# Optimization experiments

Hardware: AMD Instinct MI355X
Metric: run time of the kernel (lower is better)

The kernel has to match this reference:

```python
import jax, jax.numpy as jnp
import numpy as np

N = 50000   # nodes
E = 800000  # edges
D = 64      # num_filters == hidden_channels
NG = 5      # num_gaussians (edge_attr width, unused by forward math)
NEG_SLOPE = 0.2


def setup_inputs() -> dict:
    key = jax.random.key(0)
    ks = jax.random.split(key, 16)
    s = 1.0 / np.sqrt(D)
    return {
        "x": jax.random.normal(ks[0], (N, D), dtype=jnp.float32),
        "edge_index": jax.random.randint(ks[1], (2, E), 0, N, dtype=jnp.int64),
        "edge_weight": jax.random.uniform(ks[2], (E,), dtype=jnp.float32),
        "edge_attr": jax.random.normal(ks[3], (E, NG), dtype=jnp.float32),
        "W0": jax.random.normal(ks[4], (D, D), dtype=jnp.float32) * s,
        "b0": jnp.zeros((D,), dtype=jnp.float32),
        "W1": jax.random.normal(ks[5], (D, D), dtype=jnp.float32) * s,
        "as1": jax.random.normal(ks[6], (D,), dtype=jnp.float32) * s,
        "ad1": jax.random.normal(ks[7], (D,), dtype=jnp.float32) * s,
        "b1": jnp.zeros((D,), dtype=jnp.float32),
        "W2": jax.random.normal(ks[8], (D, D), dtype=jnp.float32) * s,
        "as2": jax.random.normal(ks[9], (D,), dtype=jnp.float32) * s,
        "ad2": jax.random.normal(ks[10], (D,), dtype=jnp.float32) * s,
        "b2": jnp.zeros((D,), dtype=jnp.float32),
    }


def gat_layer(h, src, dst, W, a_src, a_dst, b):
    # PyG GATConv, heads=1, add_self_loops=False
    hx = h @ W  # [N, D]
    # per-node attention logits, gathered per edge (edge j->i: src=j, dst=i)
    alpha = (hx * a_src).sum(-1)[src] + (hx * a_dst).sum(-1)[dst]  # [E]
    alpha = jax.nn.leaky_relu(alpha, NEG_SLOPE)
    # segment softmax grouped by destination node
    m = jax.ops.segment_max(alpha, dst, num_segments=N)
    e = jnp.exp(alpha - m[dst])
    s = jax.ops.segment_sum(e, dst, num_segments=N)
    p = e / s[dst]  # [E]
    # scatter-add weighted source features
    out = jax.ops.segment_sum(hx[src] * p[:, None], dst, num_segments=N)
    return out + b


def reference(x, edge_index, edge_weight, edge_attr,
              W0, b0, W1, as1, ad1, b1, W2, as2, ad2, b2):
    # edge_weight / edge_attr are accepted but unused, as in the torch module
    src, dst = edge_index[0], edge_index[1]
    out = jax.nn.relu(x @ W0 + b0)
    out = out + jax.nn.relu(gat_layer(out, src, dst, W1, as1, ad1, b1))
    out = out + jax.nn.relu(gat_layer(out, src, dst, W2, as2, ad2, b2))
    return out
```

## Files before the change

### kernel.cpp

```cpp
#include <hip/hip_runtime.h>

#define DD 64
#define NEG_SLOPE 0.2f
#define HS 68
#define CAP 64
#define BSH 8
#define BN  256
#define NBMAX 256
#define NBLK 256
#define CAPB 6144
#define STAGE_CAP 6144
#define AMM_NODES 32
#define CWS 65

__device__ __forceinline__ unsigned short f2bf(float f)
{
    unsigned u = __float_as_uint(f);
    u += 0x7FFFu + ((u >> 16) & 1u);
    return (unsigned short)(u >> 16);
}
__device__ __forceinline__ float bf2f(unsigned short b)
{
    return __uint_as_float(((unsigned)b) << 16);
}

__device__ __forceinline__ int wave_incl_scan(int v, int lane)
{
#pragma unroll
    for (int off = 1; off < 64; off <<= 1) {
        int t = __shfl_up(v, off);
        if (lane >= off) v += t;
    }
    return v;
}

__device__ __forceinline__ void group_aggregate(
    const ushort4* __restrict__ hx, const int* __restrict__ col,
    const float* __restrict__ sarr, float adi, int beg, int deg, int fl,
    uint2* __restrict__ cw, float4& acc, float& s)
{
    s = 0.f;
    acc = float4{0.f, 0.f, 0.f, 0.f};

#define GATH(P) { float wv = __uint_as_float((P).y);                          \
                  ushort4 uu = hx[(P).x * 16 + fl];                           \
                  acc.x += wv * bf2f(uu.x); acc.y += wv * bf2f(uu.y);         \
                  acc.z += wv * bf2f(uu.z); acc.w += wv * bf2f(uu.w); }

    if (deg <= CAP) {
        int c0 = 0, c1 = 0, c2 = 0, c3 = 0;
        float w0 = 0.f, w1 = 0.f, w2 = 0.f, w3 = 0.f;
        if (fl < deg)      { c0 = col[beg + fl];      float a = sarr[c0] + adi; a = a > 0.f ? a : NEG_SLOPE * a; w0 = __expf(a); }
        if (fl + 16 < deg) { c1 = col[beg + fl + 16]; float a = sarr[c1] + adi; a = a > 0.f ? a : NEG_SLOPE * a; w1 = __expf(a); }
        if (fl + 32 < deg) { c2 = col[beg + fl + 32]; float a = sarr[c2] + adi; a = a > 0.f ? a : NEG_SLOPE * a; w2 = __expf(a); }
        if (fl + 48 < deg) { c3 = col[beg + fl + 48]; float a = sarr[c3] + adi; a = a > 0.f ? a : NEG_SLOPE * a; w3 = __expf(a); }
        s = (w0 + w1) + (w2 + w3);

        int degR = (deg + 7) & ~7;
        if (fl < degR)      { uint2 e; e.x = (unsigned)c0; e.y = __float_as_uint(w0); cw[fl] = e; }
        if (fl + 16 < degR) { uint2 e; e.x = (unsigned)c1; e.y = __float_as_uint(w1); cw[fl + 16] = e; }
        if (fl + 32 < degR) { uint2 e; e.x = (unsigned)c2; e.y = __float_as_uint(w2); cw[fl + 32] = e; }
        if (fl + 48 < degR) { uint2 e; e.x = (unsigned)c3; e.y = __float_as_uint(w3); cw[fl + 48] = e; }

        for (int i = 0; i < degR; i += 8) {
            uint2 p0 = cw[i],     p1 = cw[i + 1], p2 = cw[i + 2], p3 = cw[i + 3];
            uint2 p4 = cw[i + 4], p5 = cw[i + 5], p6 = cw[i + 6], p7 = cw[i + 7];
            GATH(p0); GATH(p1); GATH(p2); GATH(p3);
            GATH(p4); GATH(p5); GATH(p6); GATH(p7);
        }
    } else {
        for (int base = 0; base < deg; base += 16) {
            int i = base + fl;
            uint2 e; e.x = 0u; e.y = 0u;
            if (i < deg) {
                int c = col[beg + i];
                float a = sarr[c] + adi;
                a = a > 0.f ? a : NEG_SLOPE * a;
                float wv = __expf(a);
                e.x = (unsigned)c; e.y = __float_as_uint(wv);
                s += wv;
            }
            cw[fl] = e;
#pragma unroll
            for (int j = 0; j < 16; j += 8) {
                uint2 p0 = cw[j],     p1 = cw[j + 1], p2 = cw[j + 2], p3 = cw[j + 3];
                uint2 p4 = cw[j + 4], p5 = cw[j + 5], p6 = cw[j + 6], p7 = cw[j + 7];
                GATH(p0); GATH(p1); GATH(p2); GATH(p3);
                GATH(p4); GATH(p5); GATH(p6); GATH(p7);
            }
        }
    }
#pragma unroll
    for (int off = 8; off; off >>= 1) s += __shfl_xor(s, off);
#undef GATH
}

__global__ __launch_bounds__(512) void scatter_mm(
    const int4* __restrict__ dst4, const int4* __restrict__ src4,
    const int* __restrict__ dst, const int* __restrict__ src,
    int* __restrict__ gcur, int* __restrict__ ebuf,
    int NB, int E4, int E, int C4,
    const float* __restrict__ x, const float* __restrict__ W0,
    const float* __restrict__ b0, const float* __restrict__ W1,
    const float* __restrict__ a_src, const float* __restrict__ a_dst,
    float* __restrict__ h, ushort4* __restrict__ hxb4,
    float* __restrict__ sarr, float* __restrict__ darr, int n)
{
    __shared__ float smem[DD * DD + DD * HS];
    int tid = threadIdx.x;

    if (blockIdx.x < NBLK) {
        int* lh   = (int*)smem;
        int* lcur = lh + NBMAX;
        int k = blockIdx.x;
        for (int i = tid; i < NB; i += 512) lh[i] = 0;
        __syncthreads();
        int i0 = k * C4, i1 = min(i0 + C4, E4);
        for (int i = i0 + tid; i < i1; i += 512) {
            int4 d = dst4[i];
            atomicAdd(&lh[d.x >> BSH], 1);
            atomicAdd(&lh[d.y >> BSH], 1);
            atomicAdd(&lh[d.z >> BSH], 1);
            atomicAdd(&lh[d.w >> BSH], 1);
        }
        if (k == NBLK - 1) {
            for (int e = E4 * 4 + tid; e < E; e += 512)
                atomicAdd(&lh[dst[e] >> BSH], 1);
        }
        __syncthreads();
        for (int b = tid; b < NB; b += 512) {
            int c = lh[b];
            lcur[b] = b * CAPB + (c ? atomicAdd(&gcur[b], c) : 0);
        }
        __syncthreads();
        for (int i = i0 + tid; i < i1; i += 512) {
            int4 d = dst4[i];
            int4 s = src4[i];
            int b, p;
            b = d.x >> BSH; p = atomicAdd(&lcur[b], 1);
            if (p < b * CAPB + CAPB) ebuf[p] = ((d.x & (BN - 1)) << 24) | s.x;
            b = d.y >> BSH; p = atomicAdd(&lcur[b], 1);
            if (p < b * CAPB + CAPB) ebuf[p] = ((d.y & (BN - 1)) << 24) | s.y;
            b = d.z >> BSH; p = atomicAdd(&lcur[b], 1);
            if (p < b * CAPB + CAPB) ebuf[p] = ((d.z & (BN - 1)) << 24) | s.z;
            b = d.w >> BSH; p = atomicAdd(&lcur[b], 1);
            if (p < b * CAPB + CAPB) ebuf[p] = ((d.w & (BN - 1)) << 24) | s.w;
        }
        if (k == NBLK - 1) {
            for (int e = E4 * 4 + tid; e < E; e += 512) {
                int d = dst[e];
                int b = d >> BSH;
                int p = atomicAdd(&lcur[b], 1);
                if (p < b * CAPB + CAPB)
                    ebuf[p] = ((d & (BN - 1)) << 24) | src[e];
            }
        }
        return;
    }

    float* Wsh = smem;
    float* Hsh = smem + DD * DD;
    int fg = tid & 15, ng = tid >> 4;
    int tile0 = (blockIdx.x - NBLK) * 64;

    for (int i = tid * 4; i < DD * DD; i += 2048)
        *(float4*)&Wsh[i] = *(const float4*)&W0[i];
    for (int p = 0; p < 2; ++p) {
        int nl = p * 32 + ng, gn = tile0 + nl;
        if (gn < n)
            *(float4*)&Hsh[nl * HS + 4 * fg] = *(const float4*)&x[gn * DD + 4 * fg];
    }
    __syncthreads();

    float4 acc[2];
#pragma unroll
    for (int j = 0; j < 2; ++j) acc[j] = float4{0.f, 0.f, 0.f, 0.f};
#pragma unroll 8
    for (int k = 0; k < DD; ++k) {
        float4 w4 = *(float4*)&Wsh[k * DD + 4 * fg];
#pragma unroll
        for (int j = 0; j < 2; ++j) {
            float hv = Hsh[(2 * ng + j) * HS + k];
            acc[j].x += hv * w4.x; acc[j].y += hv * w4.y;
            acc[j].z += hv * w4.z; acc[j].w += hv * w4.w;
        }
    }

    float4 b4 = *(const float4*)&b0[4 * fg];
    float4 o[2];
#pragma unroll
    for (int j = 0; j < 2; ++j) {
        o[j].x = fmaxf(acc[j].x + b4.x, 0.f);
        o[j].y = fmaxf(acc[j].y + b4.y, 0.f);
        o[j].z = fmaxf(acc[j].z + b4.z, 0.f);
        o[j].w = fmaxf(acc[j].w + b4.w, 0.f);
        int gn = tile0 + 2 * ng + j;
        if (gn < n) *(float4*)&h[gn * DD + 4 * fg] = o[j];
    }
    __syncthreads();

#pragma unroll
    for (int j = 0; j < 2; ++j)
        *(float4*)&Hsh[(2 * ng + j) * HS + 4 * fg] = o[j];
    for (int i = tid * 4; i < DD * DD; i += 2048)
        *(float4*)&Wsh[i] = *(const float4*)&W1[i];
    __syncthreads();

#pragma unroll
    for (int j = 0; j < 2; ++j) acc[j] = float4{0.f, 0.f, 0.f, 0.f};
#pragma unroll 8
    for (int k = 0; k < DD; ++k) {
        float4 w4 = *(float4*)&Wsh[k * DD + 4 * fg];
#pragma unroll
        for (int j = 0; j < 2; ++j) {
            float hv = Hsh[(2 * ng + j) * HS + k];
            acc[j].x += hv * w4.x; acc[j].y += hv * w4.y;
            acc[j].z += hv * w4.z; acc[j].w += hv * w4.w;
        }
    }

    float4 as4 = *(const float4*)&a_src[4 * fg];
    float4 ad4 = *(const float4*)&a_dst[4 * fg];
#pragma unroll
    for (int j = 0; j < 2; ++j) {
        int gn = tile0 + 2 * ng + j;
        if (gn < n) {
            ushort4 hb;
            hb.x = f2bf(acc[j].x); hb.y = f2bf(acc[j].y);
            hb.z = f2bf(acc[j].z); hb.w = f2bf(acc[j].w);
            hxb4[gn * 16 + fg] = hb;
        }
        float ps = acc[j].x * as4.x + acc[j].y * as4.y + acc[j].z * as4.z + acc[j].w * as4.w;
        float pd = acc[j].x * ad4.x + acc[j].y * ad4.y + acc[j].z * ad4.z + acc[j].w * ad4.w;
#pragma unroll
        for (int off = 8; off; off >>= 1) {
            ps += __shfl_xor(ps, off);
            pd += __shfl_xor(pd, off);
        }
        if (fg == 0 && gn < n) { sarr[gn] = ps; darr[gn] = pd; }
    }
}

__global__ __launch_bounds__(512) void group_build(
    const int* __restrict__ ebuf, const int* __restrict__ gcur,
    int* __restrict__ row_beg, int* __restrict__ degarr,
    int* __restrict__ col, int N)
{
    __shared__ int lcnt[BN];
    __shared__ int loff[BN];
    __shared__ int lcur[BN];
    __shared__ int wsum[4];
    __shared__ int stage[STAGE_CAP];
    int b = blockIdx.x, tid = threadIdx.x;
    int e0 = b * CAPB;
    int total = min(gcur[b], CAPB);
    int e1 = e0 + total;
    if (tid < BN) { lcnt[tid] = 0; lcur[tid] = 0; }
    __syncthreads();
    for (int e = e0 + tid; e < e1; e += 512)
        atomicAdd(&lcnt[((unsigned)ebuf[e]) >> 24], 1);
    __syncthreads();
    int lane = tid & 63, w = tid >> 6;
    int v = (tid < BN) ? lcnt[tid] : 0;
    int incl = wave_incl_scan(v, lane);
    if (tid < BN && lane == 63) wsum[w] = incl;
    __syncthreads();
    if (tid < BN) {
        int wo = 0;
        for (int i = 0; i < w; ++i) wo += wsum[i];
        int excl = wo + incl - v;
        loff[tid] = excl;
        int node = b * BN + tid;
        if (node < N) { row_beg[node] = e0 + excl; degarr[node] = v; }
    }
    __syncthreads();
    for (int e = e0 + tid; e < e1; e += 512) {
        int p = ebuf[e];
        int dl = ((unsigned)p) >> 24;
        int r = atomicAdd(&lcur[dl], 1);
        stage[loff[dl] + r] = p & 0xFFFFFF;
    }
    __syncthreads();
    for (int i = tid; i < total; i += 512)
        col[e0 + i] = stage[i];
}

__global__ __launch_bounds__(512) void agg_mm(
    const ushort4* __restrict__ hxA, const int* __restrict__ row_beg,
    const int* __restrict__ degarr, const int* __restrict__ col,
    const float* __restrict__ sA, const float* __restrict__ dA,
    const float* __restrict__ bias,
    float* __restrict__ h, const float* __restrict__ W,
    const float* __restrict__ a_src, const float* __restrict__ a_dst,
    ushort4* __restrict__ hxB, float* __restrict__ sB, float* __restrict__ dB,
    int n)
{
    __shared__ float Wsh[DD * DD];
    __shared__ uint2 cwbuf[AMM_NODES][CWS];
    float* Hsh = (float*)&cwbuf[0][0];

    int tid = threadIdx.x;
    int w = tid >> 6, lane = tid & 63, grp = lane >> 4, fl = lane & 15;
    int nl = 4 * w + grp;
    int tile0 = blockIdx.x * AMM_NODES;
    int v = tile0 + nl;
    bool alive = v < n;

    for (int i = tid * 4; i < DD * DD; i += 2048)
        *(float4*)&Wsh[i] = *(const float4*)&W[i];

    int beg = 0, deg = 0;
    float adi = 0.f;
    if (alive) {
        beg = row_beg[v];
        deg = degarr[v];
        adi = dA[v];
    }

    float4 acc; float s;
    group_aggregate(hxA, col, sA, adi, beg, deg, fl, &cwbuf[nl][0], acc, s);

    float4 resid = float4{0.f, 0.f, 0.f, 0.f};
    {
        float inv = (s > 0.f) ? 1.f / s : 0.f;
        float4 b4 = ((const float4*)bias)[fl];
        float4 o;
        o.x = fmaxf(acc.x * inv + b4.x, 0.f);
        o.y = fmaxf(acc.y * inv + b4.y, 0.f);
        o.z = fmaxf(acc.z * inv + b4.z, 0.f);
        o.w = fmaxf(acc.w * inv + b4.w, 0.f);
        if (alive) {
            float4* hp = (float4*)&h[v * DD + 4 * fl];
            float4 cur = *hp;
            cur.x += o.x; cur.y += o.y; cur.z += o.z; cur.w += o.w;
            *hp = cur;
            resid = cur;
        }
    }
    __syncthreads();
    *(float4*)&Hsh[nl * HS + 4 * fl] = resid;
    __syncthreads();

    int nl2 = tid >> 4;
    int fg = tid & 15;
    float4 acc2 = float4{0.f, 0.f, 0.f, 0.f};
#pragma unroll 8
    for (int k = 0; k < DD; ++k) {
        float4 w4 = *(float4*)&Wsh[k * DD + 4 * fg];
        float hv = Hsh[nl2 * HS + k];
        acc2.x += hv * w4.x; acc2.y += hv * w4.y;
        acc2.z += hv * w4.z; acc2.w += hv * w4.w;
    }
    int gn = tile0 + nl2;
    float4 as4 = *(const float4*)&a_src[4 * fg];
    float4 ad4 = *(const float4*)&a_dst[4 * fg];
    if (gn < n) {
        ushort4 hb;
        hb.x = f2bf(acc2.x); hb.y = f2bf(acc2.y);
        hb.z = f2bf(acc2.z); hb.w = f2bf(acc2.w);
        hxB[gn * 16 + fg] = hb;
    }
    float ps = acc2.x * as4.x + acc2.y * as4.y + acc2.z * as4.z + acc2.w * as4.w;
    float pd = acc2.x * ad4.x + acc2.y * ad4.y + acc2.z * ad4.z + acc2.w * ad4.w;
#pragma unroll
    for (int off = 8; off; off >>= 1) {
        ps += __shfl_xor(ps, off);
        pd += __shfl_xor(pd, off);
    }
    if (fg == 0 && gn < n) { sB[gn] = ps; dB[gn] = pd; }
}

__global__ __launch_bounds__(512) void aggregate(
    const ushort4* __restrict__ hxb4, const int* __restrict__ row_beg,
    const int* __restrict__ degarr, const int* __restrict__ col,
    const float* __restrict__ sarr, const float* __restrict__ darr,
    const float* __restrict__ bias, float* __restrict__ h, int n)
{
    __shared__ uint2 cwbuf[AMM_NODES][CWS];
    int tid = threadIdx.x;
    int w = tid >> 6, lane = tid & 63, grp = lane >> 4, fl = lane & 15;
    int nl = 4 * w + grp;
    int v = blockIdx.x * AMM_NODES + nl;
    bool alive = v < n;

    int beg = 0, deg = 0;
    float adi = 0.f;
    if (alive) {
        beg = row_beg[v];
        deg = degarr[v];
        adi = darr[v];
    }

    float4 acc; float s;
    group_aggregate(hxb4, col, sarr, adi, beg, deg, fl, &cwbuf[nl][0], acc, s);

    if (alive) {
        float inv = (s > 0.f) ? 1.f / s : 0.f;
        float4 b4 = ((const float4*)bias)[fl];
        float4 o;
        o.x = fmaxf(acc.x * inv + b4.x, 0.f);
        o.y = fmaxf(acc.y * inv + b4.y, 0.f);
        o.z = fmaxf(acc.z * inv + b4.z, 0.f);
        o.w = fmaxf(acc.w * inv + b4.w, 0.f);
        float4* hp = (float4*)&h[v * DD + 4 * fl];
        float4 cur = *hp;
        cur.x += o.x; cur.y += o.y; cur.z += o.z; cur.w += o.w;
        *hp = cur;
    }
}

extern "C" void kernel_launch(void* const* d_in, const int* in_sizes, int n_in,
                              void* d_out, int out_size, void* d_ws, size_t ws_size,
                              hipStream_t stream)
{
    const float* x  = (const float*)d_in[0];
    const int*   ei = (const int*)d_in[1];
    const float* W0 = (const float*)d_in[4];
    const float* b0 = (const float*)d_in[5];
    const float* W1 = (const float*)d_in[6];
    const float* as1= (const float*)d_in[7];
    const float* ad1= (const float*)d_in[8];
    const float* b1 = (const float*)d_in[9];
    const float* W2 = (const float*)d_in[10];
    const float* as2= (const float*)d_in[11];
    const float* ad2= (const float*)d_in[12];
    const float* b2 = (const float*)d_in[13];

    int N = in_sizes[0] / DD;
    int E = in_sizes[1] / 2;
    int E4 = E >> 2;
    int C4 = (E4 + NBLK - 1) / NBLK;
    int NB = (N + BN - 1) >> BSH;
    float* h = (float*)d_out;

    ushort4* hxA  = (ushort4*)d_ws;
    ushort4* hxB  = hxA + (size_t)N * 16;
    float* sA     = (float*)(hxB + (size_t)N * 16);
    float* dA     = sA + N;
    float* sB     = dA + N;
    float* dB     = sB + N;
    int*   row_beg= (int*)(dB + N);
    int*   degarr = row_beg + N;
    int*   gcur   = degarr + N;
    int*   ebuf   = gcur + NB;
    int*   colb   = ebuf + (size_t)NB * CAPB;

    const int* src = ei;
    const int* dst = ei + E;
    const int4* dst4 = (const int4*)dst;
    const int4* src4 = (const int4*)src;

    int tiles     = (N + 63) / 64;
    int agg_blks  = (N + AMM_NODES - 1) / AMM_NODES;

    hipMemsetAsync(gcur, 0, NB * sizeof(int), stream);
    scatter_mm<<<NBLK + tiles, 512, 0, stream>>>(
        dst4, src4, dst, src, gcur, ebuf, NB, E4, E, C4,
        x, W0, b0, W1, as1, ad1, h, hxA, sA, dA, N);
    group_build<<<NB, 512, 0, stream>>>(ebuf, gcur, row_beg, degarr, colb, N);
    agg_mm<<<agg_blks, 512, 0, stream>>>(hxA, row_beg, degarr, colb, sA, dA, b1,
                                         h, W2, as2, ad2, hxB, sB, dB, N);
    aggregate<<<agg_blks, 512, 0, stream>>>(hxB, row_beg, degarr, colb, sB, dB, b2, h, N);
}
```

Measured before the change: 179.0 us.

## Fuse CSR bucket build into first aggregation kernel with claim/done flags

Removes the separate group_build launch. The first block to reach each destination bucket claims it via atomicCAS, builds its CSR slice in shared memory and publishes a done flag, while other blocks needing that bucket spin-wait on the flag. Each aggregation block now handles two node tiles and reuses one shared buffer for staging, edge weights and the matmul tile. The stage buffer is shrunk and gains a direct-to-global fallback, and the gather tail drops the padded 8-wide loop. This saves a kernel launch and a global sync, at the cost of spin-waiting that depends on co-residency and ordering of blocks.

```diff
diff --git a/kernel.cpp b/kernel.cpp
--- a/kernel.cpp
+++ b/kernel.cpp
@@ -9,9 +9,10 @@
 #define NBMAX 256
 #define NBLK 256
 #define CAPB 6144
-#define STAGE_CAP 6144
+#define STAGE_CAP 4608
 #define AMM_NODES 32
 #define CWS 65
+#define UBYTES 21536
 
 __device__ __forceinline__ unsigned short f2bf(float f)
 {
@@ -56,18 +57,24 @@
         if (fl + 48 < deg) { c3 = col[beg + fl + 48]; float a = sarr[c3] + adi; a = a > 0.f ? a : NEG_SLOPE * a; w3 = __expf(a); }
         s = (w0 + w1) + (w2 + w3);
 
-        int degR = (deg + 7) & ~7;
-        if (fl < degR)      { uint2 e; e.x = (unsigned)c0; e.y = __float_as_uint(w0); cw[fl] = e; }
-        if (fl + 16 < degR) { uint2 e; e.x = (unsigned)c1; e.y = __float_as_uint(w1); cw[fl + 16] = e; }
-        if (fl + 32 < degR) { uint2 e; e.x = (unsigned)c2; e.y = __float_as_uint(w2); cw[fl + 32] = e; }
-        if (fl + 48 < degR) { uint2 e; e.x = (unsigned)c3; e.y = __float_as_uint(w3); cw[fl + 48] = e; }
-
-        for (int i = 0; i < degR; i += 8) {
+        if (fl < deg)      { uint2 e; e.x = (unsigned)c0; e.y = __float_as_uint(w0); cw[fl] = e; }
+        if (fl + 16 < deg) { uint2 e; e.x = (unsigned)c1; e.y = __float_as_uint(w1); cw[fl + 16] = e; }
+        if (fl + 32 < deg) { uint2 e; e.x = (unsigned)c2; e.y = __float_as_uint(w2); cw[fl + 32] = e; }
+        if (fl + 48 < deg) { uint2 e; e.x = (unsigned)c3; e.y = __float_as_uint(w3); cw[fl + 48] = e; }
+
+        int i = 0;
+        for (; i + 8 <= deg; i += 8) {
             uint2 p0 = cw[i],     p1 = cw[i + 1], p2 = cw[i + 2], p3 = cw[i + 3];
             uint2 p4 = cw[i + 4], p5 = cw[i + 5], p6 = cw[i + 6], p7 = cw[i + 7];
             GATH(p0); GATH(p1); GATH(p2); GATH(p3);
             GATH(p4); GATH(p5); GATH(p6); GATH(p7);
         }
+        if (i + 4 <= deg) {
+            uint2 p0 = cw[i], p1 = cw[i + 1], p2 = cw[i + 2], p3 = cw[i + 3];
+            GATH(p0); GATH(p1); GATH(p2); GATH(p3);
+            i += 4;
+        }
+        for (; i < deg; ++i) { uint2 p = cw[i]; GATH(p); }
     } else {
         for (int base = 0; base < deg; base += 16) {
             int i = base + fl;
@@ -241,17 +248,12 @@
     }
 }
 
-__global__ __launch_bounds__(512) void group_build(
-    const int* __restrict__ ebuf, const int* __restrict__ gcur,
-    int* __restrict__ row_beg, int* __restrict__ degarr,
-    int* __restrict__ col, int N)
-{
-    __shared__ int lcnt[BN];
-    __shared__ int loff[BN];
-    __shared__ int lcur[BN];
-    __shared__ int wsum[4];
-    __shared__ int stage[STAGE_CAP];
-    int b = blockIdx.x, tid = threadIdx.x;
+__device__ __forceinline__ void build_bucket(
+    int b, const int* __restrict__ ebuf, const int* __restrict__ gcur,
+    int* __restrict__ row_beg, int* __restrict__ degarr, int* __restrict__ col,
+    int N, int* stage, int* lcnt, int* loff, int* lcur, int* wsum)
+{
+    int tid = threadIdx.x;
     int e0 = b * CAPB;
     int total = min(gcur[b], CAPB);
     int e1 = e0 + total;
@@ -274,100 +276,156 @@
         if (node < N) { row_beg[node] = e0 + excl; degarr[node] = v; }
     }
     __syncthreads();
-    for (int e = e0 + tid; e < e1; e += 512) {
-        int p = ebuf[e];
-        int dl = ((unsigned)p) >> 24;
-        int r = atomicAdd(&lcur[dl], 1);
-        stage[loff[dl] + r] = p & 0xFFFFFF;
-    }
-    __syncthreads();
-    for (int i = tid; i < total; i += 512)
-        col[e0 + i] = stage[i];
-}
-
-__global__ __launch_bounds__(512) void agg_mm(
-    const ushort4* __restrict__ hxA, const int* __restrict__ row_beg,
-    const int* __restrict__ degarr, const int* __restrict__ col,
+    if (total <= STAGE_CAP) {
+        for (int e = e0 + tid; e < e1; e += 512) {
+            int p = ebuf[e];
+            int dl = ((unsigned)p) >> 24;
+            int r = atomicAdd(&lcur[dl], 1);
+            stage[loff[dl] + r] = p & 0xFFFFFF;
+        }
+        __syncthreads();
+        for (int i = tid; i < total; i += 512)
+            col[e0 + i] = stage[i];
+    } else {
+        for (int e = e0 + tid; e < e1; e += 512) {
+            int p = ebuf[e];
+            int dl = ((unsigned)p) >> 24;
+            int r = atomicAdd(&lcur[dl], 1);
+            col[e0 + loff[dl] + r] = p & 0xFFFFFF;
+        }
+    }
+    __syncthreads();
+}
+
+__global__ __launch_bounds__(512) void agg_mm_gb(
+    const int* __restrict__ ebuf, const int* __restrict__ gcur,
+    int* __restrict__ claim, int* __restrict__ done,
+    int* __restrict__ row_beg, int* __restrict__ degarr, int* __restrict__ col,
+    const ushort4* __restrict__ hxA,
     const float* __restrict__ sA, const float* __restrict__ dA,
     const float* __restrict__ bias,
     float* __restrict__ h, const float* __restrict__ W,
     const float* __restrict__ a_src, const float* __restrict__ a_dst,
     ushort4* __restrict__ hxB, float* __restrict__ sB, float* __restrict__ dB,
-    int n)
+    int n, int ntiles)
 {
     __shared__ float Wsh[DD * DD];
-    __shared__ uint2 cwbuf[AMM_NODES][CWS];
-    float* Hsh = (float*)&cwbuf[0][0];
-
+    __shared__ __align__(16) char ubuf[UBYTES];
+    __shared__ int mode_sh;
     int tid = threadIdx.x;
-    int w = tid >> 6, lane = tid & 63, grp = lane >> 4, fl = lane & 15;
-    int nl = 4 * w + grp;
-    int tile0 = blockIdx.x * AMM_NODES;
-    int v = tile0 + nl;
-    bool alive = v < n;
 
     for (int i = tid * 4; i < DD * DD; i += 2048)
         *(float4*)&Wsh[i] = *(const float4*)&W[i];
 
-    int beg = 0, deg = 0;
-    float adi = 0.f;
-    if (alive) {
-        beg = row_beg[v];
-        deg = degarr[v];
-        adi = dA[v];
-    }
-
-    float4 acc; float s;
-    group_aggregate(hxA, col, sA, adi, beg, deg, fl, &cwbuf[nl][0], acc, s);
-
-    float4 resid = float4{0.f, 0.f, 0.f, 0.f};
-    {
-        float inv = (s > 0.f) ? 1.f / s : 0.f;
-        float4 b4 = ((const float4*)bias)[fl];
-        float4 o;
-        o.x = fmaxf(acc.x * inv + b4.x, 0.f);
-        o.y = fmaxf(acc.y * inv + b4.y, 0.f);
-        o.z = fmaxf(acc.z * inv + b4.z, 0.f);
-        o.w = fmaxf(acc.w * inv + b4.w, 0.f);
+    int t0 = 2 * blockIdx.x;
+    if (t0 >= ntiles) return;
+    int bkt = (t0 * AMM_NODES) >> BSH;
+
+    if (tid == 0) {
+        int m = 0;
+        if (__hip_atomic_load(&done[bkt], __ATOMIC_ACQUIRE,
+                              __HIP_MEMORY_SCOPE_AGENT) == 0) {
+            m = (atomicCAS(&claim[bkt], 0, 1) == 0) ? 1 : 2;
+        }
+        mode_sh = m;
+    }
+    __syncthreads();
+    int mode = mode_sh;
+    if (mode == 1) {
+        int* stage = (int*)ubuf;
+        int* lcnt  = stage + STAGE_CAP;
+        int* loff  = lcnt + BN;
+        int* lcur  = loff + BN;
+        int* wsum  = lcur + BN;
+        build_bucket(bkt, ebuf, gcur, row_beg, degarr, col, n,
+                     stage, lcnt, loff, lcur, wsum);
+        if (tid == 0) {
+            __threadfence();
+            __hip_atomic_store(&done[bkt], 1, __ATOMIC_RELEASE,
+                               __HIP_MEMORY_SCOPE_AGENT);
+        }
+    } else if (mode == 2) {
+        if (tid == 0) {
+            while (__hip_atomic_load(&done[bkt], __ATOMIC_ACQUIRE,
+                                     __HIP_MEMORY_SCOPE_AGENT) == 0)
+                __builtin_amdgcn_s_sleep(32);
+        }
+        __syncthreads();
+    }
+    __syncthreads();
+
+    uint2* cwbuf = (uint2*)ubuf;
+    float* Hsh   = (float*)ubuf;
+    int w = tid >> 6, lane = tid & 63, grp = lane >> 4, fl = lane & 15;
+
+    int tend = min(t0 + 2, ntiles);
+    for (int t = t0; t < tend; ++t) {
+        int tile0 = t * AMM_NODES;
+        int nl = 4 * w + grp;
+        int v = tile0 + nl;
+        bool alive = v < n;
+
+        int beg = 0, deg = 0;
+        float adi = 0.f;
         if (alive) {
-            float4* hp = (float4*)&h[v * DD + 4 * fl];
-            float4 cur = *hp;
-            cur.x += o.x; cur.y += o.y; cur.z += o.z; cur.w += o.w;
-            *hp = cur;
-            resid = cur;
-        }
-    }
-    __syncthreads();
-    *(float4*)&Hsh[nl * HS + 4 * fl] = resid;
-    __syncthreads();
-
-    int nl2 = tid >> 4;
-    int fg = tid & 15;
-    float4 acc2 = float4{0.f, 0.f, 0.f, 0.f};
+            beg = row_beg[v];
+            deg = degarr[v];
+            adi = dA[v];
+        }
+
+        float4 acc; float s;
+        group_aggregate(hxA, col, sA, adi, beg, deg, fl, &cwbuf[nl * CWS], acc, s);
+
+        float4 resid = float4{0.f, 0.f, 0.f, 0.f};
+        {
+            float inv = (s > 0.f) ? 1.f / s : 0.f;
+            float4 b4 = ((const float4*)bias)[fl];
+            float4 o;
+            o.x = fmaxf(acc.x * inv + b4.x, 0.f);
+            o.y = fmaxf(acc.y * inv + b4.y, 0.f);
+            o.z = fmaxf(acc.z * inv + b4.z, 0.f);
+            o.w = fmaxf(acc.w * inv + b4.w, 0.f);
+            if (alive) {
+                float4* hp = (float4*)&h[v * DD + 4 * fl];
+                float4 cur = *hp;
+                cur.x += o.x; cur.y += o.y; cur.z += o.z; cur.w += o.w;
+                *hp = cur;
+                resid = cur;
+            }
+        }
+        __syncthreads();
+        *(float4*)&Hsh[nl * HS + 4 * fl] = resid;
+        __syncthreads();
+
+        int nl2 = tid >> 4;
+        int fg = tid & 15;
+        float4 acc2 = float4{0.f, 0.f, 0.f, 0.f};
 #pragma unroll 8
-    for (int k = 0; k < DD; ++k) {
-        float4 w4 = *(float4*)&Wsh[k * DD + 4 * fg];
-        float hv = Hsh[nl2 * HS + k];
-        acc2.x += hv * w4.x; acc2.y += hv * w4.y;
-        acc2.z += hv * w4.z; acc2.w += hv * w4.w;
-    }
-    int gn = tile0 + nl2;
-    float4 as4 = *(const float4*)&a_src[4 * fg];
-    float4 ad4 = *(const float4*)&a_dst[4 * fg];
-    if (gn < n) {
-        ushort4 hb;
-        hb.x = f2bf(acc2.x); hb.y = f2bf(acc2.y);
-        hb.z = f2bf(acc2.z); hb.w = f2bf(acc2.w);
-        hxB[gn * 16 + fg] = hb;
-    }
-    float ps = acc2.x * as4.x + acc2.y * as4.y + acc2.z * as4.z + acc2.w * as4.w;
-    float pd = acc2.x * ad4.x + acc2.y * ad4.y + acc2.z * ad4.z + acc2.w * ad4.w;
-#pragma unroll
-    for (int off = 8; off; off >>= 1) {
-        ps += __shfl_xor(ps, off);
-        pd += __shfl_xor(pd, off);
-    }
-    if (fg == 0 && gn < n) { sB[gn] = ps; dB[gn] = pd; }
+        for (int k = 0; k < DD; ++k) {
+            float4 w4 = *(float4*)&Wsh[k * DD + 4 * fg];
+            float hv = Hsh[nl2 * HS + k];
+            acc2.x += hv * w4.x; acc2.y += hv * w4.y;
+            acc2.z += hv * w4.z; acc2.w += hv * w4.w;
+        }
+        int gn = tile0 + nl2;
+        float4 as4 = *(const float4*)&a_src[4 * fg];
+        float4 ad4 = *(const float4*)&a_dst[4 * fg];
+        if (gn < n) {
+            ushort4 hb;
+            hb.x = f2bf(acc2.x); hb.y = f2bf(acc2.y);
+            hb.z = f2bf(acc2.z); hb.w = f2bf(acc2.w);
+            hxB[gn * 16 + fg] = hb;
+        }
+        float ps = acc2.x * as4.x + acc2.y * as4.y + acc2.z * as4.z + acc2.w * as4.w;
+        float pd = acc2.x * ad4.x + acc2.y * ad4.y + acc2.z * ad4.z + acc2.w * ad4.w;
+#pragma unroll
+        for (int off = 8; off; off >>= 1) {
+            ps += __shfl_xor(ps, off);
+            pd += __shfl_xor(pd, off);
+        }
+        if (fg == 0 && gn < n) { sB[gn] = ps; dB[gn] = pd; }
+        __syncthreads();
+    }
 }
 
 __global__ __launch_bounds__(512) void aggregate(
@@ -442,7 +500,9 @@
     int*   row_beg= (int*)(dB + N);
     int*   degarr = row_beg + N;
     int*   gcur   = degarr + N;
-    int*   ebuf   = gcur + NB;
+    int*   claim  = gcur + NB;
+    int*   done   = claim + NB;
+    int*   ebuf   = done + NB;
     int*   colb   = ebuf + (size_t)NB * CAPB;
 
     const int* src = ei;
@@ -450,15 +510,18 @@
     const int4* dst4 = (const int4*)dst;
     const int4* src4 = (const int4*)src;
 
-    int tiles     = (N + 63) / 64;
-    int agg_blks  = (N + AMM_NODES - 1) / AMM_NODES;
-
-    hipMemsetAsync(gcur, 0, NB * sizeof(int), stream);
+    int tiles   = (N + 63) / 64;
+    int ntiles  = (N + AMM_NODES - 1) / AMM_NODES;
+    int aggblks = (ntiles + 1) / 2;
+    int fagblks = ntiles;
+
+    hipMemsetAsync(gcur, 0, 3 * NB * sizeof(int), stream);
     scatter_mm<<<NBLK + tiles, 512, 0, stream>>>(
         dst4, src4, dst, src, gcur, ebuf, NB, E4, E, C4,
         x, W0, b0, W1, as1, ad1, h, hxA, sA, dA, N);
-    group_build<<<NB, 512, 0, stream>>>(ebuf, gcur, row_beg, degarr, colb, N);
-    agg_mm<<<agg_blks, 512, 0, stream>>>(hxA, row_beg, degarr, colb, sA, dA, b1,
-                                         h, W2, as2, ad2, hxB, sB, dB, N);
-    aggregate<<<agg_blks, 512, 0, stream>>>(hxB, row_beg, degarr, colb, sB, dB, b2, h, N);
-}
+    agg_mm_gb<<<aggblks, 512, 0, stream>>>(
+        ebuf, gcur, claim, done, row_beg, degarr, colb,
+        hxA, sA, dA, b1, h, W2, as2, ad2, hxB, sB, dB, N, ntiles);
+    aggregate<<<fagblks, 512, 0, stream>>>(hxB, row_beg, degarr, colb,
+                                           sB, dB, b2, h, N);
+}
```

Measured after the change: 250.3 us. 39.9% more time.

## Fuse all stages into one persistent cooperative kernel with grid syncs

Applied to the files above, without the earlier changes.

Merges the memset, scatter/matmul, group build, first aggregate+matmul, and final aggregate kernels into a single cooperative persistent kernel that loops over work units and separates phases with grid.sync(). This removes four launch boundaries and the memset launch. In exchange, each phase runs on a grid capped by occupancy and pays for grid-wide barriers. The single kernel uses one shared-memory buffer sized for the largest phase and launch_bounds(512,8), which may limit registers or occupancy.

```diff
diff --git a/kernel.cpp b/kernel.cpp
--- a/kernel.cpp
+++ b/kernel.cpp
@@ -1,4 +1,7 @@
 #include <hip/hip_runtime.h>
+#include <hip/hip_cooperative_groups.h>
+
+namespace cg = cooperative_groups;
 
 #define DD 64
 #define NEG_SLOPE 0.2f
@@ -12,6 +15,7 @@
 #define STAGE_CAP 6144
 #define AMM_NODES 32
 #define CWS 65
+#define SMEM_BYTES 34816
 
 __device__ __forceinline__ unsigned short f2bf(float f)
 {
@@ -95,73 +99,72 @@
 #undef GATH
 }
 
-__global__ __launch_bounds__(512) void scatter_mm(
-    const int4* __restrict__ dst4, const int4* __restrict__ src4,
+__device__ __forceinline__ void scatter_role(
+    int k, const int4* __restrict__ dst4, const int4* __restrict__ src4,
     const int* __restrict__ dst, const int* __restrict__ src,
     int* __restrict__ gcur, int* __restrict__ ebuf,
-    int NB, int E4, int E, int C4,
-    const float* __restrict__ x, const float* __restrict__ W0,
+    int NB, int E4, int E, int C4, char* smem)
+{
+    int tid = threadIdx.x;
+    int* lh   = (int*)smem;
+    int* lcur = lh + NBMAX;
+    for (int i = tid; i < NB; i += 512) lh[i] = 0;
+    __syncthreads();
+    int i0 = k * C4, i1 = min(i0 + C4, E4);
+    for (int i = i0 + tid; i < i1; i += 512) {
+        int4 d = dst4[i];
+        atomicAdd(&lh[d.x >> BSH], 1);
+        atomicAdd(&lh[d.y >> BSH], 1);
+        atomicAdd(&lh[d.z >> BSH], 1);
+        atomicAdd(&lh[d.w >> BSH], 1);
+    }
+    if (k == NBLK - 1) {
+        for (int e = E4 * 4 + tid; e < E; e += 512)
+            atomicAdd(&lh[dst[e] >> BSH], 1);
+    }
+    __syncthreads();
+    for (int b = tid; b < NB; b += 512) {
+        int c = lh[b];
+        lcur[b] = b * CAPB + (c ? atomicAdd(&gcur[b], c) : 0);
+    }
+    __syncthreads();
+    for (int i = i0 + tid; i < i1; i += 512) {
+        int4 d = dst4[i];
+        int4 s = src4[i];
+        int b, p;
+        b = d.x >> BSH; p = atomicAdd(&lcur[b], 1);
+        if (p < b * CAPB + CAPB) ebuf[p] = ((d.x & (BN - 1)) << 24) | s.x;
+        b = d.y >> BSH; p = atomicAdd(&lcur[b], 1);
+        if (p < b * CAPB + CAPB) ebuf[p] = ((d.y & (BN - 1)) << 24) | s.y;
+        b = d.z >> BSH; p = atomicAdd(&lcur[b], 1);
+        if (p < b * CAPB + CAPB) ebuf[p] = ((d.z & (BN - 1)) << 24) | s.z;
+        b = d.w >> BSH; p = atomicAdd(&lcur[b], 1);
+        if (p < b * CAPB + CAPB) ebuf[p] = ((d.w & (BN - 1)) << 24) | s.w;
+    }
+    if (k == NBLK - 1) {
+        for (int e = E4 * 4 + tid; e < E; e += 512) {
+            int d = dst[e];
+            int b = d >> BSH;
+            int p = atomicAdd(&lcur[b], 1);
+            if (p < b * CAPB + CAPB)
+                ebuf[p] = ((d & (BN - 1)) << 24) | src[e];
+        }
+    }
+    __syncthreads();
+}
+
+__device__ __forceinline__ void mm_role(
+    int tileIdx, const float* __restrict__ x, const float* __restrict__ W0,
     const float* __restrict__ b0, const float* __restrict__ W1,
     const float* __restrict__ a_src, const float* __restrict__ a_dst,
     float* __restrict__ h, ushort4* __restrict__ hxb4,
-    float* __restrict__ sarr, float* __restrict__ darr, int n)
-{
-    __shared__ float smem[DD * DD + DD * HS];
+    float* __restrict__ sarr, float* __restrict__ darr, int n, char* smem)
+{
     int tid = threadIdx.x;
-
-    if (blockIdx.x < NBLK) {
-        int* lh   = (int*)smem;
-        int* lcur = lh + NBMAX;
-        int k = blockIdx.x;
-        for (int i = tid; i < NB; i += 512) lh[i] = 0;
-        __syncthreads();
-        int i0 = k * C4, i1 = min(i0 + C4, E4);
-        for (int i = i0 + tid; i < i1; i += 512) {
-            int4 d = dst4[i];
-            atomicAdd(&lh[d.x >> BSH], 1);
-            atomicAdd(&lh[d.y >> BSH], 1);
-            atomicAdd(&lh[d.z >> BSH], 1);
-            atomicAdd(&lh[d.w >> BSH], 1);
-        }
-        if (k == NBLK - 1) {
-            for (int e = E4 * 4 + tid; e < E; e += 512)
-                atomicAdd(&lh[dst[e] >> BSH], 1);
-        }
-        __syncthreads();
-        for (int b = tid; b < NB; b += 512) {
-            int c = lh[b];
-            lcur[b] = b * CAPB + (c ? atomicAdd(&gcur[b], c) : 0);
-        }
-        __syncthreads();
-        for (int i = i0 + tid; i < i1; i += 512) {
-            int4 d = dst4[i];
-            int4 s = src4[i];
-            int b, p;
-            b = d.x >> BSH; p = atomicAdd(&lcur[b], 1);
-            if (p < b * CAPB + CAPB) ebuf[p] = ((d.x & (BN - 1)) << 24) | s.x;
-            b = d.y >> BSH; p = atomicAdd(&lcur[b], 1);
-            if (p < b * CAPB + CAPB) ebuf[p] = ((d.y & (BN - 1)) << 24) | s.y;
-            b = d.z >> BSH; p = atomicAdd(&lcur[b], 1);
-            if (p < b * CAPB + CAPB) ebuf[p] = ((d.z & (BN - 1)) << 24) | s.z;
-            b = d.w >> BSH; p = atomicAdd(&lcur[b], 1);
-            if (p < b * CAPB + CAPB) ebuf[p] = ((d.w & (BN - 1)) << 24) | s.w;
-        }
-        if (k == NBLK - 1) {
-            for (int e = E4 * 4 + tid; e < E; e += 512) {
-                int d = dst[e];
-                int b = d >> BSH;
-                int p = atomicAdd(&lcur[b], 1);
-                if (p < b * CAPB + CAPB)
-                    ebuf[p] = ((d & (BN - 1)) << 24) | src[e];
-            }
-        }
-        return;
-    }
-
-    float* Wsh = smem;
-    float* Hsh = smem + DD * DD;
+    float* Wsh = (float*)smem;
+    float* Hsh = Wsh + DD * DD;
     int fg = tid & 15, ng = tid >> 4;
-    int tile0 = (blockIdx.x - NBLK) * 64;
+    int tile0 = tileIdx * 64;
 
     for (int i = tid * 4; i < DD * DD; i += 2048)
         *(float4*)&Wsh[i] = *(const float4*)&W0[i];
@@ -239,19 +242,20 @@
         }
         if (fg == 0 && gn < n) { sarr[gn] = ps; darr[gn] = pd; }
     }
-}
-
-__global__ __launch_bounds__(512) void group_build(
-    const int* __restrict__ ebuf, const int* __restrict__ gcur,
+    __syncthreads();
+}
+
+__device__ __forceinline__ void gb_role(
+    int b, const int* __restrict__ ebuf, const int* __restrict__ gcur,
     int* __restrict__ row_beg, int* __restrict__ degarr,
-    int* __restrict__ col, int N)
-{
-    __shared__ int lcnt[BN];
-    __shared__ int loff[BN];
-    __shared__ int lcur[BN];
-    __shared__ int wsum[4];
-    __shared__ int stage[STAGE_CAP];
-    int b = blockIdx.x, tid = threadIdx.x;
+    int* __restrict__ col, int N, char* smem)
+{
+    int tid = threadIdx.x;
+    int* stage = (int*)smem;
+    int* lcnt  = stage + STAGE_CAP;
+    int* loff  = lcnt + BN;
+    int* lcur  = loff + BN;
+    int* wsum  = lcur + BN;
     int e0 = b * CAPB;
     int total = min(gcur[b], CAPB);
     int e1 = e0 + total;
@@ -283,129 +287,145 @@
     __syncthreads();
     for (int i = tid; i < total; i += 512)
         col[e0 + i] = stage[i];
-}
-
-__global__ __launch_bounds__(512) void agg_mm(
-    const ushort4* __restrict__ hxA, const int* __restrict__ row_beg,
-    const int* __restrict__ degarr, const int* __restrict__ col,
-    const float* __restrict__ sA, const float* __restrict__ dA,
-    const float* __restrict__ bias,
-    float* __restrict__ h, const float* __restrict__ W,
-    const float* __restrict__ a_src, const float* __restrict__ a_dst,
-    ushort4* __restrict__ hxB, float* __restrict__ sB, float* __restrict__ dB,
-    int n)
-{
-    __shared__ float Wsh[DD * DD];
-    __shared__ uint2 cwbuf[AMM_NODES][CWS];
-    float* Hsh = (float*)&cwbuf[0][0];
-
+    __syncthreads();
+}
+
+__global__ __launch_bounds__(512, 8) void fused_all(
+    const int4* dst4, const int4* src4, const int* dst, const int* src,
+    int* gcur, int* ebuf, int NB, int E4, int E, int C4,
+    const float* x, const float* W0, const float* b0, const float* W1,
+    const float* as1, const float* ad1, const float* b1,
+    const float* W2, const float* as2, const float* ad2, const float* b2,
+    float* h, ushort4* hxA, float* sA, float* dA,
+    ushort4* hxB, float* sB, float* dB,
+    int* row_beg, int* degarr, int* col,
+    int n, int tiles, int ntiles)
+{
+    cg::grid_group grid = cg::this_grid();
+    __shared__ __align__(16) char smem[SMEM_BYTES];
     int tid = threadIdx.x;
-    int w = tid >> 6, lane = tid & 63, grp = lane >> 4, fl = lane & 15;
-    int nl = 4 * w + grp;
-    int tile0 = blockIdx.x * AMM_NODES;
-    int v = tile0 + nl;
-    bool alive = v < n;
-
-    for (int i = tid * 4; i < DD * DD; i += 2048)
-        *(float4*)&Wsh[i] = *(const float4*)&W[i];
-
-    int beg = 0, deg = 0;
-    float adi = 0.f;
-    if (alive) {
-        beg = row_beg[v];
-        deg = degarr[v];
-        adi = dA[v];
-    }
-
-    float4 acc; float s;
-    group_aggregate(hxA, col, sA, adi, beg, deg, fl, &cwbuf[nl][0], acc, s);
-
-    float4 resid = float4{0.f, 0.f, 0.f, 0.f};
+    int nb = gridDim.x;
+
+    for (int i = blockIdx.x * 512 + tid; i < NB; i += nb * 512) gcur[i] = 0;
+    grid.sync();
+
+    int U1 = NBLK + tiles;
+    for (int u = blockIdx.x; u < U1; u += nb) {
+        if (u < NBLK)
+            scatter_role(u, dst4, src4, dst, src, gcur, ebuf, NB, E4, E, C4, smem);
+        else
+            mm_role(u - NBLK, x, W0, b0, W1, as1, ad1, h, hxA, sA, dA, n, smem);
+    }
+    grid.sync();
+
+    for (int b = blockIdx.x; b < NB; b += nb)
+        gb_role(b, ebuf, gcur, row_beg, degarr, col, n, smem);
+    grid.sync();
+
     {
-        float inv = (s > 0.f) ? 1.f / s : 0.f;
-        float4 b4 = ((const float4*)bias)[fl];
-        float4 o;
-        o.x = fmaxf(acc.x * inv + b4.x, 0.f);
-        o.y = fmaxf(acc.y * inv + b4.y, 0.f);
-        o.z = fmaxf(acc.z * inv + b4.z, 0.f);
-        o.w = fmaxf(acc.w * inv + b4.w, 0.f);
-        if (alive) {
-            float4* hp = (float4*)&h[v * DD + 4 * fl];
-            float4 cur = *hp;
-            cur.x += o.x; cur.y += o.y; cur.z += o.z; cur.w += o.w;
-            *hp = cur;
-            resid = cur;
-        }
-    }
-    __syncthreads();
-    *(float4*)&Hsh[nl * HS + 4 * fl] = resid;
-    __syncthreads();
-
-    int nl2 = tid >> 4;
-    int fg = tid & 15;
-    float4 acc2 = float4{0.f, 0.f, 0.f, 0.f};
+        float* Wsh   = (float*)smem;
+        uint2* cwbuf = (uint2*)(smem + DD * DD * 4);
+        float* Hsh   = (float*)(smem + DD * DD * 4);
+        for (int i = tid * 4; i < DD * DD; i += 2048)
+            *(float4*)&Wsh[i] = *(const float4*)&W2[i];
+        __syncthreads();
+
+        int w = tid >> 6, lane = tid & 63, grp = lane >> 4, fl = lane & 15;
+        for (int t = blockIdx.x; t < ntiles; t += nb) {
+            int tile0 = t * AMM_NODES;
+            int nl = 4 * w + grp;
+            int v = tile0 + nl;
+            bool alive = v < n;
+
+            int beg = 0, deg = 0;
+            float adi = 0.f;
+            if (alive) { beg = row_beg[v]; deg = degarr[v]; adi = dA[v]; }
+
+            float4 acc; float s;
+            group_aggregate(hxA, col, sA, adi, beg, deg, fl, &cwbuf[nl * CWS], acc, s);
+
+            float4 resid = float4{0.f, 0.f, 0.f, 0.f};
+            {
+                float inv = (s > 0.f) ? 1.f / s : 0.f;
+                float4 b4 = ((const float4*)b1)[fl];
+                float4 o;
+                o.x = fmaxf(acc.x * inv + b4.x, 0.f);
+                o.y = fmaxf(acc.y * inv + b4.y, 0.f);
+                o.z = fmaxf(acc.z * inv + b4.z, 0.f);
+                o.w = fmaxf(acc.w * inv + b4.w, 0.f);
+                if (alive) {
+                    float4* hp = (float4*)&h[v * DD + 4 * fl];
+                    float4 cur = *hp;
+                    cur.x += o.x; cur.y += o.y; cur.z += o.z; cur.w += o.w;
+                    *hp = cur;
+                    resid = cur;
+                }
+            }
+            __syncthreads();
+            *(float4*)&Hsh[nl * HS + 4 * fl] = resid;
+            __syncthreads();
+
+            int nl2 = tid >> 4;
+            int fg = tid & 15;
+            float4 acc2 = float4{0.f, 0.f, 0.f, 0.f};
 #pragma unroll 8
-    for (int k = 0; k < DD; ++k) {
-        float4 w4 = *(float4*)&Wsh[k * DD + 4 * fg];
-        float hv = Hsh[nl2 * HS + k];
-        acc2.x += hv * w4.x; acc2.y += hv * w4.y;
-        acc2.z += hv * w4.z; acc2.w += hv * w4.w;
-    }
-    int gn = tile0 + nl2;
-    float4 as4 = *(const float4*)&a_src[4 * fg];
-    float4 ad4 = *(const float4*)&a_dst[4 * fg];
-    if (gn < n) {
-        ushort4 hb;
-        hb.x = f2bf(acc2.x); hb.y = f2bf(acc2.y);
-        hb.z = f2bf(acc2.z); hb.w = f2bf(acc2.w);
-        hxB[gn * 16 + fg] = hb;
-    }
-    float ps = acc2.x * as4.x + acc2.y * as4.y + acc2.z * as4.z + acc2.w * as4.w;
-    float pd = acc2.x * ad4.x + acc2.y * ad4.y + acc2.z * ad4.z + acc2.w * ad4.w;
-#pragma unroll
-    for (int off = 8; off; off >>= 1) {
-        ps += __shfl_xor(ps, off);
-        pd += __shfl_xor(pd, off);
-    }
-    if (fg == 0 && gn < n) { sB[gn] = ps; dB[gn] = pd; }
-}
-
-__global__ __launch_bounds__(512) void aggregate(
-    const ushort4* __restrict__ hxb4, const int* __restrict__ row_beg,
-    const int* __restrict__ degarr, const int* __restrict__ col,
-    const float* __restrict__ sarr, const float* __restrict__ darr,
-    const float* __restrict__ bias, float* __restrict__ h, int n)
-{
-    __shared__ uint2 cwbuf[AMM_NODES][CWS];
-    int tid = threadIdx.x;
-    int w = tid >> 6, lane = tid & 63, grp = lane >> 4, fl = lane & 15;
-    int nl = 4 * w + grp;
-    int v = blockIdx.x * AMM_NODES + nl;
-    bool alive = v < n;
-
-    int beg = 0, deg = 0;
-    float adi = 0.f;
-    if (alive) {
-        beg = row_beg[v];
-        deg = degarr[v];
-        adi = darr[v];
-    }
-
-    float4 acc; float s;
-    group_aggregate(hxb4, col, sarr, adi, beg, deg, fl, &cwbuf[nl][0], acc, s);
-
-    if (alive) {
-        float inv = (s > 0.f) ? 1.f / s : 0.f;
-        float4 b4 = ((const float4*)bias)[fl];
-        float4 o;
-        o.x = fmaxf(acc.x * inv + b4.x, 0.f);
-        o.y = fmaxf(acc.y * inv + b4.y, 0.f);
-        o.z = fmaxf(acc.z * inv + b4.z, 0.f);
-        o.w = fmaxf(acc.w * inv + b4.w, 0.f);
-        float4* hp = (float4*)&h[v * DD + 4 * fl];
-        float4 cur = *hp;
-        cur.x += o.x; cur.y += o.y; cur.z += o.z; cur.w += o.w;
-        *hp = cur;
+            for (int k = 0; k < DD; ++k) {
+                float4 w4 = *(float4*)&Wsh[k * DD + 4 * fg];
+                float hv = Hsh[nl2 * HS + k];
+                acc2.x += hv * w4.x; acc2.y += hv * w4.y;
+                acc2.z += hv * w4.z; acc2.w += hv * w4.w;
+            }
+            int gn = tile0 + nl2;
+            float4 as4 = *(const float4*)&as2[4 * fg];
+            float4 ad4 = *(const float4*)&ad2[4 * fg];
+            if (gn < n) {
+                ushort4 hb;
+                hb.x = f2bf(acc2.x); hb.y = f2bf(acc2.y);
+                hb.z = f2bf(acc2.z); hb.w = f2bf(acc2.w);
+                hxB[gn * 16 + fg] = hb;
+            }
+            float ps = acc2.x * as4.x + acc2.y * as4.y + acc2.z * as4.z + acc2.w * as4.w;
+            float pd = acc2.x * ad4.x + acc2.y * ad4.y + acc2.z * ad4.z + acc2.w * ad4.w;
+#pragma unroll
+            for (int off = 8; off; off >>= 1) {
+                ps += __shfl_xor(ps, off);
+                pd += __shfl_xor(pd, off);
+            }
+            if (fg == 0 && gn < n) { sB[gn] = ps; dB[gn] = pd; }
+            __syncthreads();
+        }
+    }
+    grid.sync();
+
+    {
+        uint2* cwbuf = (uint2*)smem;
+        int w = tid >> 6, lane = tid & 63, grp = lane >> 4, fl = lane & 15;
+        for (int t = blockIdx.x; t < ntiles; t += nb) {
+            int nl = 4 * w + grp;
+            int v = t * AMM_NODES + nl;
+            bool alive = v < n;
+
+            int beg = 0, deg = 0;
+            float adi = 0.f;
+            if (alive) { beg = row_beg[v]; deg = degarr[v]; adi = dB[v]; }
+
+            float4 acc; float s;
+            group_aggregate(hxB, col, sB, adi, beg, deg, fl, &cwbuf[nl * CWS], acc, s);
+
+            if (alive) {
+                float inv = (s > 0.f) ? 1.f / s : 0.f;
+                float4 b4 = ((const float4*)b2)[fl];
+                float4 o;
+                o.x = fmaxf(acc.x * inv + b4.x, 0.f);
+                o.y = fmaxf(acc.y * inv + b4.y, 0.f);
+                o.z = fmaxf(acc.z * inv + b4.z, 0.f);
+                o.w = fmaxf(acc.w * inv + b4.w, 0.f);
+                float4* hp = (float4*)&h[v * DD + 4 * fl];
+                float4 cur = *hp;
+                cur.x += o.x; cur.y += o.y; cur.z += o.z; cur.w += o.w;
+                *hp = cur;
+            }
+        }
     }
 }
 
@@ -450,15 +470,26 @@
     const int4* dst4 = (const int4*)dst;
     const int4* src4 = (const int4*)src;
 
-    int tiles     = (N + 63) / 64;
-    int agg_blks  = (N + AMM_NODES - 1) / AMM_NODES;
-
-    hipMemsetAsync(gcur, 0, NB * sizeof(int), stream);
-    scatter_mm<<<NBLK + tiles, 512, 0, stream>>>(
-        dst4, src4, dst, src, gcur, ebuf, NB, E4, E, C4,
-        x, W0, b0, W1, as1, ad1, h, hxA, sA, dA, N);
-    group_build<<<NB, 512, 0, stream>>>(ebuf, gcur, row_beg, degarr, colb, N);
-    agg_mm<<<agg_blks, 512, 0, stream>>>(hxA, row_beg, degarr, colb, sA, dA, b1,
-                                         h, W2, as2, ad2, hxB, sB, dB, N);
-    aggregate<<<agg_blks, 512, 0, stream>>>(hxB, row_beg, degarr, colb, sB, dB, b2, h, N);
-}
+    int tiles  = (N + 63) / 64;
+    int ntiles = (N + AMM_NODES - 1) / AMM_NODES;
+
+    int maxActive = 0;
+    hipOccupancyMaxActiveBlocksPerMultiprocessor(&maxActive, fused_all, 512, 0);
+    if (maxActive < 1) maxActive = 1;
+    long capacity = (long)maxActive * 256;
+    int grid = (int)(capacity < ntiles ? capacity : ntiles);
+    if (grid < 1) grid = 1;
+
+    void* args[] = {
+        (void*)&dst4, (void*)&src4, (void*)&dst, (void*)&src,
+        (void*)&gcur, (void*)&ebuf, (void*)&NB, (void*)&E4, (void*)&E, (void*)&C4,
+        (void*)&x, (void*)&W0, (void*)&b0, (void*)&W1,
+        (void*)&as1, (void*)&ad1, (void*)&b1,
+        (void*)&W2, (void*)&as2, (void*)&ad2, (void*)&b2,
+        (void*)&h, (void*)&hxA, (void*)&sA, (void*)&dA,
+        (void*)&hxB, (void*)&sB, (void*)&dB,
+        (void*)&row_beg, (void*)&degarr, (void*)&colb,
+        (void*)&N, (void*)&tiles, (void*)&ntiles
+    };
+    hipLaunchCooperativeKernel(fused_all, dim3(grid), dim3(512), args, 0, stream);
+}
```

New measurement: 429.5 us. 2.4x slower.
